# Kernel optimization log

Hardware: AMD Instinct MI355X
Metric: run time of the kernel (lower is better)

## Reference

```python
import jax, jax.numpy as jnp
import numpy as np

DIM = 512
CTX = 768
GROUPS = 32
EPS = 1e-5


def setup_inputs() -> dict:
    key = jax.random.key(0)
    ks = jax.random.split(key, 12)
    B, H, W, S = 16, 64, 64, 256
    x = jax.random.normal(ks[0], (B, DIM, H, W), dtype=jnp.float32)
    context = jax.random.normal(ks[1], (B, S, CTX), dtype=jnp.float32)
    gn_w = jnp.ones((DIM,), jnp.float32)
    gn_b = jnp.zeros((DIM,), jnp.float32)
    ln_w = jnp.ones((CTX,), jnp.float32)
    ln_b = jnp.zeros((CTX,), jnp.float32)
    wq = jax.random.normal(ks[2], (DIM, DIM), jnp.float32) * (DIM ** -0.5)
    bq = jnp.zeros((DIM,), jnp.float32)
    wkv = jax.random.normal(ks[3], (2 * DIM, CTX), jnp.float32) * (CTX ** -0.5)
    bkv = jnp.zeros((2 * DIM,), jnp.float32)
    wo = jax.random.normal(ks[4], (DIM, DIM), jnp.float32) * (DIM ** -0.5)
    bo = jnp.zeros((DIM,), jnp.float32)
    return {"x": x, "context": context, "gn_w": gn_w, "gn_b": gn_b,
            "ln_w": ln_w, "ln_b": ln_b, "wq": wq, "bq": bq,
            "wkv": wkv, "bkv": bkv, "wo": wo, "bo": bo}


def reference(x, context, gn_w, gn_b, ln_w, ln_b, wq, bq, wkv, bkv, wo, bo):
    b, c, h, w = x.shape
    scale = c ** -0.5
    # GroupNorm over (channels-per-group, H, W)
    xr = x.reshape(b, GROUPS, -1)
    mu = xr.mean(-1, keepdims=True)
    var = xr.var(-1, keepdims=True)
    xn = ((xr - mu) * jax.lax.rsqrt(var + EPS)).reshape(b, c, h, w)
    xn = xn * gn_w[None, :, None, None] + gn_b[None, :, None, None]
    # 1x1 conv query projection as channel GEMM
    q = jnp.einsum('bchw,oc->bohw', xn, wq) + bq[None, :, None, None]
    q = q.reshape(b, c, h * w).transpose(0, 2, 1)  # b, hw, c
    # LayerNorm on context
    cm = context.mean(-1, keepdims=True)
    cv = context.var(-1, keepdims=True)
    cn = (context - cm) * jax.lax.rsqrt(cv + EPS) * ln_w + ln_b
    kv = cn @ wkv.T + bkv  # b, s, 2c
    k, v = jnp.split(kv, 2, axis=-1)
    sim = jnp.einsum('bic,bjc->bij', q, k) * scale
    attn = jax.nn.softmax(sim, axis=-1)
    out = jnp.einsum('bij,bjc->bic', attn, v)
    out = out.transpose(0, 2, 1).reshape(b, c, h, w)
    out = jnp.einsum('bchw,oc->bohw', out, wo) + bo[None, :, None, None]
    return out + x
```

## Files before the change

### kernel.cpp

```cpp
#include <hip/hip_runtime.h>

typedef unsigned short u16;
typedef __attribute__((ext_vector_type(8))) short short8;
typedef __attribute__((ext_vector_type(4))) float f32x4;

#define DIM 512
#define CTX 768
#define HW 4096
#define NB 16
#define NS 256
#define EPSV 1e-5f

__device__ inline u16 f2bf(float f) {
    union { float f; unsigned u; } x; x.f = f;
    unsigned r = x.u + 0x7fffu + ((x.u >> 16) & 1u);
    return (u16)(r >> 16);
}
__device__ inline float bf2f(u16 v) {
    union { unsigned u; float f; } x; x.u = (unsigned)v << 16; return x.f;
}

__global__ void gn_stats(const float* __restrict__ x, const float* __restrict__ gn_w,
                         const float* __restrict__ gn_b, float* __restrict__ ga,
                         float* __restrict__ gd) {
    const int bg = blockIdx.x;
    const int b = bg >> 5, g = bg & 31;
    const float* base = x + ((long)b * DIM + g * 16) * HW;
    float s1 = 0.f, s2 = 0.f;
    const int tid = threadIdx.x;
    for (int i = tid; i < 16384; i += 256) {
        float4 v = ((const float4*)base)[i];
        s1 += v.x + v.y + v.z + v.w;
        s2 += v.x * v.x + v.y * v.y + v.z * v.z + v.w * v.w;
    }
    __shared__ float r1[256], r2[256];
    r1[tid] = s1; r2[tid] = s2; __syncthreads();
    for (int s = 128; s > 0; s >>= 1) {
        if (tid < s) { r1[tid] += r1[tid + s]; r2[tid] += r2[tid + s]; }
        __syncthreads();
    }
    __shared__ float mu_s, rs_s;
    if (tid == 0) {
        float mu = r1[0] * (1.f / 65536.f);
        float var = r2[0] * (1.f / 65536.f) - mu * mu;
        mu_s = mu; rs_s = rsqrtf(var + EPSV);
    }
    __syncthreads();
    if (tid < 16) {
        int c = g * 16 + tid;
        float aa = rs_s * gn_w[c];
        ga[b * DIM + c] = aa;
        gd[b * DIM + c] = gn_b[c] - mu_s * aa;
    }
}

__global__ void gn_apply_t(const float* __restrict__ x, const float* __restrict__ ga,
                           const float* __restrict__ gd, u16* __restrict__ xnt) {
    const int b = blockIdx.y;
    const int c0 = (blockIdx.x & 7) * 64;
    const int p0 = (blockIdx.x >> 3) * 64;
    __shared__ u16 t[64][68];
    const int tid = threadIdx.x;
    const int tc = tid >> 4;
    const int tp = (tid & 15) * 4;
    #pragma unroll
    for (int i = 0; i < 4; i++) {
        const int c = c0 + tc + i * 16;
        const float a = ga[b * DIM + c];
        const float d = gd[b * DIM + c];
        float4 v = *(const float4*)&x[((long)b * DIM + c) * HW + p0 + tp];
        u16* dst = &t[tc + i * 16][tp];
        dst[0] = f2bf(v.x * a + d);
        dst[1] = f2bf(v.y * a + d);
        dst[2] = f2bf(v.z * a + d);
        dst[3] = f2bf(v.w * a + d);
    }
    __syncthreads();
    const int wp = tid >> 3;
    const int wc = (tid & 7) * 8;
    #pragma unroll
    for (int i = 0; i < 2; i++) {
        const int p = wp + i * 32;
        short8 o;
        #pragma unroll
        for (int k = 0; k < 8; k++) o[k] = t[wc + k][p];
        *(short8*)&xnt[((long)b * HW + p0 + p) * DIM + c0 + wc] = o;
    }
}

__global__ void ln_ctx(const float* __restrict__ ctx, const float* __restrict__ ln_w,
                       const float* __restrict__ ln_b, u16* __restrict__ cn) {
    const int row = blockIdx.x;
    const int tid = threadIdx.x;
    const float* r = ctx + (long)row * CTX;
    float v[3]; float s1 = 0.f, s2 = 0.f;
    #pragma unroll
    for (int i = 0; i < 3; i++) { v[i] = r[tid + i * 256]; s1 += v[i]; s2 += v[i] * v[i]; }
    __shared__ float r1[256], r2[256];
    r1[tid] = s1; r2[tid] = s2; __syncthreads();
    for (int s = 128; s > 0; s >>= 1) {
        if (tid < s) { r1[tid] += r1[tid + s]; r2[tid] += r2[tid + s]; }
        __syncthreads();
    }
    __shared__ float mu_s, rs_s;
    if (tid == 0) {
        float mu = r1[0] * (1.f / 768.f);
        float var = r2[0] * (1.f / 768.f) - mu * mu;
        mu_s = mu; rs_s = rsqrtf(var + EPSV);
    }
    __syncthreads();
    #pragma unroll
    for (int i = 0; i < 3; i++) {
        int idx = tid + i * 256;
        cn[(long)row * CTX + idx] = f2bf((v[i] - mu_s) * rs_s * ln_w[idx] + ln_b[idx]);
    }
}

__global__ void cvt_weights(const float* __restrict__ wq, const float* __restrict__ wkv,
                            const float* __restrict__ wo, u16* __restrict__ wqtb,
                            u16* __restrict__ wkvb, u16* __restrict__ wob) {
    int i = blockIdx.x * 256 + threadIdx.x;
    if (i < 262144) {
        wqtb[(i & 511) * 512 + (i >> 9)] = f2bf(wq[i]);
        wob[i] = f2bf(wo[i]);
    }
    if (i < 786432) wkvb[i] = f2bf(wkv[i]);
}

__global__ void kbias_k(const u16* __restrict__ k, const float* __restrict__ bq,
                        float* __restrict__ kbias) {
    const int row = blockIdx.x;
    const int tid = threadIdx.x;
    const u16* r = k + (long)row * DIM;
    float s = bf2f(r[tid]) * bq[tid] + bf2f(r[tid + 256]) * bq[tid + 256];
    __shared__ float red[256];
    red[tid] = s; __syncthreads();
    for (int st = 128; st > 0; st >>= 1) {
        if (tid < st) red[tid] += red[tid + st];
        __syncthreads();
    }
    if (tid == 0) kbias[row] = red[0];
}

__launch_bounds__(256, 2)
__global__ void gemm_kv(const u16* __restrict__ A, const u16* __restrict__ Bm,
                        const float* __restrict__ bias,
                        u16* __restrict__ outk, u16* __restrict__ outv) {
    __shared__ u16 As[128][56];
    __shared__ u16 Bs[128][56];
    const int tid = threadIdx.x;
    const int lane = tid & 63;
    const int wave = tid >> 6;
    const int bb = blockIdx.y;
    const int m0 = (blockIdx.x >> 3) << 7;
    const int n0 = (blockIdx.x & 7) << 7;
    const u16* Ab = A + (long)bb * NS * CTX + (long)m0 * CTX;
    const u16* Bb = Bm + (long)n0 * CTX;

    const int sr = tid >> 2;
    const int sc = (tid & 3) << 3;
    const int l16 = lane & 15;
    const int quad = lane >> 4;
    const int wr = (wave >> 1) << 6;
    const int wc = (wave & 1) << 6;

    const u16* Ap0 = Ab + (long)sr * CTX + sc;
    const u16* Ap1 = Ab + (long)(sr + 64) * CTX + sc;
    const u16* Bp0 = Bb + (long)sr * CTX + sc;
    const u16* Bp1 = Bb + (long)(sr + 64) * CTX + sc;
    short8 rA0 = *(const short8*)Ap0;
    short8 rA1 = *(const short8*)Ap1;
    short8 rB0 = *(const short8*)Bp0;
    short8 rB1 = *(const short8*)Bp1;

    f32x4 acc[4][4] = {};
    for (int k0 = 0; k0 < CTX; k0 += 32) {
        if (k0) __syncthreads();
        *(short8*)&As[sr][sc]      = rA0;
        *(short8*)&As[sr + 64][sc] = rA1;
        *(short8*)&Bs[sr][sc]      = rB0;
        *(short8*)&Bs[sr + 64][sc] = rB1;
        __syncthreads();
        if (k0 + 32 < CTX) {
            rA0 = *(const short8*)(Ap0 + k0 + 32);
            rA1 = *(const short8*)(Ap1 + k0 + 32);
            rB0 = *(const short8*)(Bp0 + k0 + 32);
            rB1 = *(const short8*)(Bp1 + k0 + 32);
        }
        short8 af[4], bfr[4];
        #pragma unroll
        for (int i = 0; i < 4; i++) af[i] = *(const short8*)&As[wr + i * 16 + l16][quad * 8];
        #pragma unroll
        for (int j = 0; j < 4; j++) bfr[j] = *(const short8*)&Bs[wc + j * 16 + l16][quad * 8];
        #pragma unroll
        for (int i = 0; i < 4; i++)
            #pragma unroll
            for (int j = 0; j < 4; j++)
                acc[i][j] = __builtin_amdgcn_mfma_f32_16x16x32_bf16(af[i], bfr[j], acc[i][j], 0, 0, 0);
    }

    #pragma unroll
    for (int i = 0; i < 4; i++) {
        #pragma unroll
        for (int r = 0; r < 4; r++) {
            const int row = m0 + wr + i * 16 + quad * 4 + r;
            #pragma unroll
            for (int j = 0; j < 4; j++) {
                const int col = n0 + wc + j * 16 + l16;
                float v = acc[i][j][r] + bias[col];
                if (col < DIM) outk[(long)bb * NS * DIM + (long)row * DIM + col] = f2bf(v);
                else           outv[(long)bb * NS * DIM + (long)row * DIM + (col - DIM)] = f2bf(v);
            }
        }
    }
}

__launch_bounds__(256, 2)
__global__ void gemm_qv(const u16* __restrict__ kb_, const u16* __restrict__ vb_,
                        const u16* __restrict__ wqtb, const u16* __restrict__ wob,
                        u16* __restrict__ Kq, u16* __restrict__ Vot) {
    __shared__ u16 As[128][56];
    __shared__ u16 Bs[128][56];
    const int tid = threadIdx.x;
    const int lane = tid & 63;
    const int wave = tid >> 6;
    const int bb = blockIdx.y;
    const bool isV = blockIdx.z != 0;
    const int m0 = (blockIdx.x >> 2) << 7;
    const int n0 = (blockIdx.x & 3) << 7;
    const u16* Ab = (isV ? vb_ : kb_) + (long)bb * NS * DIM + (long)m0 * DIM;
    const u16* Bb = (isV ? wob : wqtb) + (long)n0 * DIM;

    const int sr = tid >> 2;
    const int sc = (tid & 3) << 3;
    const int l16 = lane & 15;
    const int quad = lane >> 4;
    const int wr = (wave >> 1) << 6;
    const int wc = (wave & 1) << 6;

    const u16* Ap0 = Ab + (long)sr * DIM + sc;
    const u16* Ap1 = Ab + (long)(sr + 64) * DIM + sc;
    const u16* Bp0 = Bb + (long)sr * DIM + sc;
    const u16* Bp1 = Bb + (long)(sr + 64) * DIM + sc;
    short8 rA0 = *(const short8*)Ap0;
    short8 rA1 = *(const short8*)Ap1;
    short8 rB0 = *(const short8*)Bp0;
    short8 rB1 = *(const short8*)Bp1;

    f32x4 acc[4][4] = {};
    for (int k0 = 0; k0 < DIM; k0 += 32) {
        if (k0) __syncthreads();
        *(short8*)&As[sr][sc]      = rA0;
        *(short8*)&As[sr + 64][sc] = rA1;
        *(short8*)&Bs[sr][sc]      = rB0;
        *(short8*)&Bs[sr + 64][sc] = rB1;
        __syncthreads();
        if (k0 + 32 < DIM) {
            rA0 = *(const short8*)(Ap0 + k0 + 32);
            rA1 = *(const short8*)(Ap1 + k0 + 32);
            rB0 = *(const short8*)(Bp0 + k0 + 32);
            rB1 = *(const short8*)(Bp1 + k0 + 32);
        }
        short8 af[4], bfr[4];
        #pragma unroll
        for (int i = 0; i < 4; i++) af[i] = *(const short8*)&As[wr + i * 16 + l16][quad * 8];
        #pragma unroll
        for (int j = 0; j < 4; j++) bfr[j] = *(const short8*)&Bs[wc + j * 16 + l16][quad * 8];
        #pragma unroll
        for (int i = 0; i < 4; i++)
            #pragma unroll
            for (int j = 0; j < 4; j++)
                acc[i][j] = __builtin_amdgcn_mfma_f32_16x16x32_bf16(af[i], bfr[j], acc[i][j], 0, 0, 0);
    }

    #pragma unroll
    for (int i = 0; i < 4; i++) {
        #pragma unroll
        for (int r = 0; r < 4; r++) {
            const int row = m0 + wr + i * 16 + quad * 4 + r;
            #pragma unroll
            for (int j = 0; j < 4; j++) {
                const int col = n0 + wc + j * 16 + l16;
                const u16 v = f2bf(acc[i][j][r]);
                if (!isV) Kq[(long)bb * NS * DIM + (long)row * DIM + col] = v;
                else      Vot[(long)bb * DIM * NS + (long)col * NS + row] = v;
            }
        }
    }
}

__launch_bounds__(512, 4)
__global__ void flash_attn(const u16* __restrict__ xnt, const u16* __restrict__ Kq,
                           const u16* __restrict__ Vot, const float* __restrict__ kbias,
                           const float* __restrict__ bo, const float* __restrict__ x,
                           float* __restrict__ out) {
    __shared__ __align__(16) char fsm[69632];
    u16 (*As)[56]      = (u16(*)[56])(fsm);
    u16 (*Bs)[56]      = (u16(*)[56])(fsm + 14336);
    u16 (*P)[264]      = (u16(*)[264])(fsm);
    float (*red)[4]    = (float(*)[4])(fsm + 67584);

    const int tid = threadIdx.x;
    const int lane = tid & 63;
    const int wave = tid >> 6;
    const int mw = wave >> 2;
    const int nw = wave & 3;
    const int l16 = lane & 15;
    const int quad = lane >> 4;
    const int b = blockIdx.y;
    const int m0 = blockIdx.x << 7;

    const u16* Ab = xnt + ((long)b * HW + m0) * DIM;
    const u16* Bb = Kq + (long)b * NS * DIM;

    const int rS = tid >> 2, cS = (tid & 3) << 3;
    const int rB = tid >> 1, cB = (tid & 1) << 4;
    const u16* Ap = Ab + (long)rS * DIM + cS;
    const u16* Bp = Bb + (long)rB * DIM + cB;
    short8 rA  = *(const short8*)(Ap);
    short8 rB0 = *(const short8*)(Bp);
    short8 rB1 = *(const short8*)(Bp + 8);

    f32x4 acc[4][4] = {};
    for (int k0 = 0; k0 < DIM; k0 += 32) {
        if (k0) __syncthreads();
        *(short8*)&As[rS][cS]     = rA;
        *(short8*)&Bs[rB][cB]     = rB0;
        *(short8*)&Bs[rB][cB + 8] = rB1;
        __syncthreads();
        if (k0 + 32 < DIM) {
            rA  = *(const short8*)(Ap + k0 + 32);
            rB0 = *(const short8*)(Bp + k0 + 32);
            rB1 = *(const short8*)(Bp + k0 + 40);
        }
        short8 af[4], bfr[4];
        #pragma unroll
        for (int i = 0; i < 4; i++) af[i] = *(const short8*)&As[mw * 64 + i * 16 + l16][quad * 8];
        #pragma unroll
        for (int j = 0; j < 4; j++) bfr[j] = *(const short8*)&Bs[nw * 64 + j * 16 + l16][quad * 8];
        #pragma unroll
        for (int i = 0; i < 4; i++)
            #pragma unroll
            for (int j = 0; j < 4; j++)
                acc[i][j] = __builtin_amdgcn_mfma_f32_16x16x32_bf16(af[i], bfr[j], acc[i][j], 0, 0, 0);
    }

    const float scale = 0.044194173824159216f;
    float kb[4];
    #pragma unroll
    for (int j = 0; j < 4; j++) kb[j] = kbias[b * NS + nw * 64 + j * 16 + l16];

    #pragma unroll
    for (int i = 0; i < 4; i++) {
        #pragma unroll
        for (int r = 0; r < 4; r++) {
            float m = -1e30f;
            #pragma unroll
            for (int j = 0; j < 4; j++) {
                float v = (acc[i][j][r] + kb[j]) * scale;
                acc[i][j][r] = v;
                m = fmaxf(m, v);
            }
            #pragma unroll
            for (int off = 1; off < 16; off <<= 1) m = fmaxf(m, __shfl_xor(m, off));
            if (l16 == 0) red[mw * 64 + i * 16 + quad * 4 + r][nw] = m;
        }
    }
    __syncthreads();
    float rsum[4][4];
    #pragma unroll
    for (int i = 0; i < 4; i++) {
        #pragma unroll
        for (int r = 0; r < 4; r++) {
            const int row = mw * 64 + i * 16 + quad * 4 + r;
            float4 rv = *(const float4*)red[row];
            float gm = fmaxf(fmaxf(rv.x, rv.y), fmaxf(rv.z, rv.w));
            float s = 0.f;
            #pragma unroll
            for (int j = 0; j < 4; j++) {
                float e = __expf(acc[i][j][r] - gm);
                acc[i][j][r] = e;
                s += e;
            }
            #pragma unroll
            for (int off = 1; off < 16; off <<= 1) s += __shfl_xor(s, off);
            rsum[i][r] = s;
        }
    }
    __syncthreads();
    #pragma unroll
    for (int i = 0; i < 4; i++)
        #pragma unroll
        for (int r = 0; r < 4; r++)
            if (l16 == 0) red[mw * 64 + i * 16 + quad * 4 + r][nw] = rsum[i][r];
    __syncthreads();
    #pragma unroll
    for (int i = 0; i < 4; i++) {
        #pragma unroll
        for (int r = 0; r < 4; r++) {
            const int row = mw * 64 + i * 16 + quad * 4 + r;
            float4 sv = *(const float4*)red[row];
            float inv = 1.f / (sv.x + sv.y + sv.z + sv.w);
            #pragma unroll
            for (int j = 0; j < 4; j++)
                P[row][nw * 64 + j * 16 + l16] = f2bf(acc[i][j][r] * inv);
        }
    }
    __syncthreads();

    const u16* Vb = Vot + ((long)b * DIM + nw * 32 + l16) * NS + quad * 8;
    for (int nc = 0; nc < 4; nc++) {
        f32x4 oacc[4][2];
        #pragma unroll
        for (int i = 0; i < 4; i++)
            #pragma unroll
            for (int jj = 0; jj < 2; jj++)
                oacc[i][jj] = (f32x4){0.f, 0.f, 0.f, 0.f};
        #pragma unroll
        for (int kk = 0; kk < 8; kk++) {
            short8 pf[4], vf[2];
            #pragma unroll
            for (int i = 0; i < 4; i++)
                pf[i] = *(const short8*)&P[mw * 64 + i * 16 + l16][kk * 32 + quad * 8];
            #pragma unroll
            for (int jj = 0; jj < 2; jj++)
                vf[jj] = *(const short8*)(Vb + (long)(nc * 128 + jj * 16) * NS + kk * 32);
            #pragma unroll
            for (int i = 0; i < 4; i++)
                #pragma unroll
                for (int jj = 0; jj < 2; jj++)
                    oacc[i][jj] = __builtin_amdgcn_mfma_f32_16x16x32_bf16(pf[i], vf[jj], oacc[i][jj], 0, 0, 0);
        }
        #pragma unroll
        for (int jj = 0; jj < 2; jj++) {
            const int c = nc * 128 + nw * 32 + jj * 16 + l16;
            const float bv = bo[c];
            const long base = ((long)b * DIM + c) * HW + m0 + mw * 64 + quad * 4;
            #pragma unroll
            for (int i = 0; i < 4; i++) {
                float4 xv = *(const float4*)&x[base + i * 16];
                float4 o;
                o.x = oacc[i][jj][0] + xv.x + bv;
                o.y = oacc[i][jj][1] + xv.y + bv;
                o.z = oacc[i][jj][2] + xv.z + bv;
                o.w = oacc[i][jj][3] + xv.w + bv;
                *(float4*)&out[base + i * 16] = o;
            }
        }
    }
}

extern "C" void kernel_launch(void* const* d_in, const int* in_sizes, int n_in,
                              void* d_out, int out_size, void* d_ws, size_t ws_size,
                              hipStream_t stream) {
    const float* x    = (const float*)d_in[0];
    const float* ctx  = (const float*)d_in[1];
    const float* gn_w = (const float*)d_in[2];
    const float* gn_b = (const float*)d_in[3];
    const float* ln_w = (const float*)d_in[4];
    const float* ln_b = (const float*)d_in[5];
    const float* wq   = (const float*)d_in[6];
    const float* bq   = (const float*)d_in[7];
    const float* wkv  = (const float*)d_in[8];
    const float* bkv  = (const float*)d_in[9];
    const float* wo   = (const float*)d_in[10];
    const float* bo   = (const float*)d_in[11];

    char* ws = (char*)d_ws;
    u16*   xnt  = (u16*)(ws + 0);
    u16*   cn   = (u16*)(ws + 67108864);
    u16*   kb_  = (u16*)(ws + 73400320);
    u16*   vb_  = (u16*)(ws + 77594624);
    u16*   Kq   = (u16*)(ws + 81788928);
    u16*   Vot  = (u16*)(ws + 85983232);
    u16*   wqtb = (u16*)(ws + 90177536);
    u16*   wkvb = (u16*)(ws + 90701824);
    u16*   wob  = (u16*)(ws + 92274688);
    float* ga   = (float*)(ws + 92798976);
    float* gd   = ga + NB * DIM;
    float* kbias = (float*)(ws + 92864512);

    gn_stats<<<dim3(NB * 32), dim3(256), 0, stream>>>(x, gn_w, gn_b, ga, gd);
    gn_apply_t<<<dim3(512, NB), dim3(256), 0, stream>>>(x, ga, gd, xnt);
    ln_ctx<<<dim3(NB * NS), dim3(256), 0, stream>>>(ctx, ln_w, ln_b, cn);
    cvt_weights<<<dim3(3072), dim3(256), 0, stream>>>(wq, wkv, wo, wqtb, wkvb, wob);

    gemm_kv<<<dim3(2 * 8, NB), dim3(256), 0, stream>>>(cn, wkvb, bkv, kb_, vb_);
    gemm_qv<<<dim3(2 * 4, NB, 2), dim3(256), 0, stream>>>(kb_, vb_, wqtb, wob, Kq, Vot);
    kbias_k<<<dim3(NB * NS), dim3(256), 0, stream>>>(kb_, bq, kbias);
    flash_attn<<<dim3(32, NB), dim3(512), 0, stream>>>(
        xnt, Kq, Vot, kbias, bo, x, (float*)d_out);
}
```

Measured before the change: 450.7 us.

## Fold Wq/Wo into KV weights and restage attention epilogue through LDS

```diff
diff --git a/kernel.cpp b/kernel.cpp
--- a/kernel.cpp
+++ b/kernel.cpp
@@ -88,8 +88,55 @@
     }
 }
 
+__global__ void cvt_weights(const float* __restrict__ wq, const float* __restrict__ wkv,
+                            const float* __restrict__ wo, u16* __restrict__ wqtb,
+                            u16* __restrict__ wkvtb, u16* __restrict__ wob) {
+    int i = blockIdx.x * 256 + threadIdx.x;
+    if (i < 262144) {
+        wqtb[(i & 511) * 512 + (i >> 9)] = f2bf(wq[i]);
+        wob[i] = f2bf(wo[i]);
+    }
+    if (i < 786432) {
+        int o = i / 768, e = i - o * 768;
+        wkvtb[e * 1024 + o] = f2bf(wkv[i]);
+    }
+}
+
+__global__ void bias_prep(const u16* __restrict__ wqtb, const u16* __restrict__ wob,
+                          const u16* __restrict__ wkvtb, const float* __restrict__ bq,
+                          const float* __restrict__ bkv, float* __restrict__ bKV,
+                          float* __restrict__ wt, float* __restrict__ c0) {
+    const int bid = blockIdx.x, tid = threadIdx.x;
+    float s = 0.f;
+    if (bid < 512) {
+        const u16* r = wqtb + (long)bid * 512;
+        s = bf2f(r[tid]) * bkv[tid] + bf2f(r[tid + 256]) * bkv[tid + 256];
+    } else if (bid < 1024) {
+        const u16* r = wob + (long)(bid - 512) * 512;
+        s = bf2f(r[tid]) * bkv[512 + tid] + bf2f(r[tid + 256]) * bkv[512 + tid + 256];
+    } else if (bid < 1792) {
+        const u16* r = wkvtb + (long)(bid - 1024) * 1024;
+        s = bf2f(r[tid]) * bq[tid] + bf2f(r[tid + 256]) * bq[tid + 256];
+    } else {
+        s = bq[tid] * bkv[tid] + bq[tid + 256] * bkv[tid + 256];
+    }
+    __shared__ float red[256];
+    red[tid] = s; __syncthreads();
+    for (int st = 128; st > 0; st >>= 1) {
+        if (tid < st) red[tid] += red[tid + st];
+        __syncthreads();
+    }
+    if (tid == 0) {
+        if (bid < 1024) bKV[bid] = red[0];
+        else if (bid < 1792) wt[bid - 1024] = red[0];
+        else *c0 = red[0];
+    }
+}
+
 __global__ void ln_ctx(const float* __restrict__ ctx, const float* __restrict__ ln_w,
-                       const float* __restrict__ ln_b, u16* __restrict__ cn) {
+                       const float* __restrict__ ln_b, const float* __restrict__ wt,
+                       const float* __restrict__ c0, u16* __restrict__ cn,
+                       float* __restrict__ kbias) {
     const int row = blockIdx.x;
     const int tid = threadIdx.x;
     const float* r = ctx + (long)row * CTX;
@@ -109,43 +156,95 @@
         mu_s = mu; rs_s = rsqrtf(var + EPSV);
     }
     __syncthreads();
+    float kb = 0.f;
     #pragma unroll
     for (int i = 0; i < 3; i++) {
         int idx = tid + i * 256;
-        cn[(long)row * CTX + idx] = f2bf((v[i] - mu_s) * rs_s * ln_w[idx] + ln_b[idx]);
-    }
-}
-
-__global__ void cvt_weights(const float* __restrict__ wq, const float* __restrict__ wkv,
-                            const float* __restrict__ wo, u16* __restrict__ wqtb,
-                            u16* __restrict__ wkvb, u16* __restrict__ wob) {
-    int i = blockIdx.x * 256 + threadIdx.x;
-    if (i < 262144) {
-        wqtb[(i & 511) * 512 + (i >> 9)] = f2bf(wq[i]);
-        wob[i] = f2bf(wo[i]);
-    }
-    if (i < 786432) wkvb[i] = f2bf(wkv[i]);
-}
-
-__global__ void kbias_k(const u16* __restrict__ k, const float* __restrict__ bq,
-                        float* __restrict__ kbias) {
-    const int row = blockIdx.x;
+        float nv = (v[i] - mu_s) * rs_s * ln_w[idx] + ln_b[idx];
+        cn[(long)row * CTX + idx] = f2bf(nv);
+        kb += nv * wt[idx];
+    }
+    r1[tid] = kb; __syncthreads();
+    for (int s = 128; s > 0; s >>= 1) {
+        if (tid < s) r1[tid] += r1[tid + s];
+        __syncthreads();
+    }
+    if (tid == 0) kbias[row] = r1[0] + *c0;
+}
+
+__launch_bounds__(256, 2)
+__global__ void gemm_wprep(const u16* __restrict__ wqtb, const u16* __restrict__ wob,
+                           const u16* __restrict__ wkvtb, u16* __restrict__ Wt) {
+    __shared__ u16 As[128][56];
+    __shared__ u16 Bs[128][56];
     const int tid = threadIdx.x;
-    const u16* r = k + (long)row * DIM;
-    float s = bf2f(r[tid]) * bq[tid] + bf2f(r[tid + 256]) * bq[tid + 256];
-    __shared__ float red[256];
-    red[tid] = s; __syncthreads();
-    for (int st = 128; st > 0; st >>= 1) {
-        if (tid < st) red[tid] += red[tid + st];
-        __syncthreads();
-    }
-    if (tid == 0) kbias[row] = red[0];
+    const int lane = tid & 63;
+    const int wave = tid >> 6;
+    const bool isV = blockIdx.z != 0;
+    const int m0 = (blockIdx.x / 6) << 7;
+    const int n0 = (blockIdx.x % 6) << 7;
+    const u16* Ab = (isV ? wob : wqtb) + (long)m0 * 512;
+    const u16* Bb = wkvtb + (long)n0 * 1024 + (isV ? 512 : 0);
+    u16* Ob = Wt + (isV ? (long)512 * 768 : 0);
+
+    const int sr = tid >> 2;
+    const int sc = (tid & 3) << 3;
+    const int l16 = lane & 15;
+    const int quad = lane >> 4;
+    const int wr = (wave >> 1) << 6;
+    const int wc = (wave & 1) << 6;
+
+    const u16* Ap0 = Ab + (long)sr * 512 + sc;
+    const u16* Ap1 = Ab + (long)(sr + 64) * 512 + sc;
+    const u16* Bp0 = Bb + (long)sr * 1024 + sc;
+    const u16* Bp1 = Bb + (long)(sr + 64) * 1024 + sc;
+    short8 rA0 = *(const short8*)Ap0;
+    short8 rA1 = *(const short8*)Ap1;
+    short8 rB0 = *(const short8*)Bp0;
+    short8 rB1 = *(const short8*)Bp1;
+
+    f32x4 acc[4][4] = {};
+    for (int k0 = 0; k0 < 512; k0 += 32) {
+        if (k0) __syncthreads();
+        *(short8*)&As[sr][sc]      = rA0;
+        *(short8*)&As[sr + 64][sc] = rA1;
+        *(short8*)&Bs[sr][sc]      = rB0;
+        *(short8*)&Bs[sr + 64][sc] = rB1;
+        __syncthreads();
+        if (k0 + 32 < 512) {
+            rA0 = *(const short8*)(Ap0 + k0 + 32);
+            rA1 = *(const short8*)(Ap1 + k0 + 32);
+            rB0 = *(const short8*)(Bp0 + k0 + 32);
+            rB1 = *(const short8*)(Bp1 + k0 + 32);
+        }
+        short8 af[4], bfr[4];
+        #pragma unroll
+        for (int i = 0; i < 4; i++) af[i] = *(const short8*)&As[wr + i * 16 + l16][quad * 8];
+        #pragma unroll
+        for (int j = 0; j < 4; j++) bfr[j] = *(const short8*)&Bs[wc + j * 16 + l16][quad * 8];
+        #pragma unroll
+        for (int i = 0; i < 4; i++)
+            #pragma unroll
+            for (int j = 0; j < 4; j++)
+                acc[i][j] = __builtin_amdgcn_mfma_f32_16x16x32_bf16(af[i], bfr[j], acc[i][j], 0, 0, 0);
+    }
+    #pragma unroll
+    for (int i = 0; i < 4; i++)
+        #pragma unroll
+        for (int r = 0; r < 4; r++) {
+            const int row = m0 + wr + i * 16 + quad * 4 + r;
+            #pragma unroll
+            for (int j = 0; j < 4; j++) {
+                const int col = n0 + wc + j * 16 + l16;
+                Ob[(long)row * 768 + col] = f2bf(acc[i][j][r]);
+            }
+        }
 }
 
 __launch_bounds__(256, 2)
-__global__ void gemm_kv(const u16* __restrict__ A, const u16* __restrict__ Bm,
-                        const float* __restrict__ bias,
-                        u16* __restrict__ outk, u16* __restrict__ outv) {
+__global__ void gemm_kvq(const u16* __restrict__ cn, const u16* __restrict__ Wt,
+                         const float* __restrict__ bKV,
+                         u16* __restrict__ Kq, u16* __restrict__ Vot) {
     __shared__ u16 As[128][56];
     __shared__ u16 Bs[128][56];
     const int tid = threadIdx.x;
@@ -154,8 +253,8 @@
     const int bb = blockIdx.y;
     const int m0 = (blockIdx.x >> 3) << 7;
     const int n0 = (blockIdx.x & 7) << 7;
-    const u16* Ab = A + (long)bb * NS * CTX + (long)m0 * CTX;
-    const u16* Bb = Bm + (long)n0 * CTX;
+    const u16* Ab = cn + (long)bb * NS * CTX + (long)m0 * CTX;
+    const u16* Bb = Wt + (long)n0 * CTX;
 
     const int sr = tid >> 2;
     const int sc = (tid & 3) << 3;
@@ -200,93 +299,18 @@
     }
 
     #pragma unroll
-    for (int i = 0; i < 4; i++) {
+    for (int i = 0; i < 4; i++)
         #pragma unroll
         for (int r = 0; r < 4; r++) {
             const int row = m0 + wr + i * 16 + quad * 4 + r;
             #pragma unroll
             for (int j = 0; j < 4; j++) {
                 const int col = n0 + wc + j * 16 + l16;
-                float v = acc[i][j][r] + bias[col];
-                if (col < DIM) outk[(long)bb * NS * DIM + (long)row * DIM + col] = f2bf(v);
-                else           outv[(long)bb * NS * DIM + (long)row * DIM + (col - DIM)] = f2bf(v);
+                const u16 v = f2bf(acc[i][j][r] + bKV[col]);
+                if (col < DIM) Kq[(long)bb * NS * DIM + (long)row * DIM + col] = v;
+                else           Vot[(long)bb * DIM * NS + (long)(col - DIM) * NS + row] = v;
             }
         }
-    }
-}
-
-__launch_bounds__(256, 2)
-__global__ void gemm_qv(const u16* __restrict__ kb_, const u16* __restrict__ vb_,
-                        const u16* __restrict__ wqtb, const u16* __restrict__ wob,
-                        u16* __restrict__ Kq, u16* __restrict__ Vot) {
-    __shared__ u16 As[128][56];
-    __shared__ u16 Bs[128][56];
-    const int tid = threadIdx.x;
-    const int lane = tid & 63;
-    const int wave = tid >> 6;
-    const int bb = blockIdx.y;
-    const bool isV = blockIdx.z != 0;
-    const int m0 = (blockIdx.x >> 2) << 7;
-    const int n0 = (blockIdx.x & 3) << 7;
-    const u16* Ab = (isV ? vb_ : kb_) + (long)bb * NS * DIM + (long)m0 * DIM;
-    const u16* Bb = (isV ? wob : wqtb) + (long)n0 * DIM;
-
-    const int sr = tid >> 2;
-    const int sc = (tid & 3) << 3;
-    const int l16 = lane & 15;
-    const int quad = lane >> 4;
-    const int wr = (wave >> 1) << 6;
-    const int wc = (wave & 1) << 6;
-
-    const u16* Ap0 = Ab + (long)sr * DIM + sc;
-    const u16* Ap1 = Ab + (long)(sr + 64) * DIM + sc;
-    const u16* Bp0 = Bb + (long)sr * DIM + sc;
-    const u16* Bp1 = Bb + (long)(sr + 64) * DIM + sc;
-    short8 rA0 = *(const short8*)Ap0;
-    short8 rA1 = *(const short8*)Ap1;
-    short8 rB0 = *(const short8*)Bp0;
-    short8 rB1 = *(const short8*)Bp1;
-
-    f32x4 acc[4][4] = {};
-    for (int k0 = 0; k0 < DIM; k0 += 32) {
-        if (k0) __syncthreads();
-        *(short8*)&As[sr][sc]      = rA0;
-        *(short8*)&As[sr + 64][sc] = rA1;
-        *(short8*)&Bs[sr][sc]      = rB0;
-        *(short8*)&Bs[sr + 64][sc] = rB1;
-        __syncthreads();
-        if (k0 + 32 < DIM) {
-            rA0 = *(const short8*)(Ap0 + k0 + 32);
-            rA1 = *(const short8*)(Ap1 + k0 + 32);
-            rB0 = *(const short8*)(Bp0 + k0 + 32);
-            rB1 = *(const short8*)(Bp1 + k0 + 32);
-        }
-        short8 af[4], bfr[4];
-        #pragma unroll
-        for (int i = 0; i < 4; i++) af[i] = *(const short8*)&As[wr + i * 16 + l16][quad * 8];
-        #pragma unroll
-        for (int j = 0; j < 4; j++) bfr[j] = *(const short8*)&Bs[wc + j * 16 + l16][quad * 8];
-        #pragma unroll
-        for (int i = 0; i < 4; i++)
-            #pragma unroll
-            for (int j = 0; j < 4; j++)
-                acc[i][j] = __builtin_amdgcn_mfma_f32_16x16x32_bf16(af[i], bfr[j], acc[i][j], 0, 0, 0);
-    }
-
-    #pragma unroll
-    for (int i = 0; i < 4; i++) {
-        #pragma unroll
-        for (int r = 0; r < 4; r++) {
-            const int row = m0 + wr + i * 16 + quad * 4 + r;
-            #pragma unroll
-            for (int j = 0; j < 4; j++) {
-                const int col = n0 + wc + j * 16 + l16;
-                const u16 v = f2bf(acc[i][j][r]);
-                if (!isV) Kq[(long)bb * NS * DIM + (long)row * DIM + col] = v;
-                else      Vot[(long)bb * DIM * NS + (long)col * NS + row] = v;
-            }
-        }
-    }
 }
 
 __launch_bounds__(512, 4)
@@ -294,11 +318,12 @@
                            const u16* __restrict__ Vot, const float* __restrict__ kbias,
                            const float* __restrict__ bo, const float* __restrict__ x,
                            float* __restrict__ out) {
-    __shared__ __align__(16) char fsm[69632];
+    __shared__ __align__(16) char fsm[78080];
     u16 (*As)[56]      = (u16(*)[56])(fsm);
     u16 (*Bs)[56]      = (u16(*)[56])(fsm + 14336);
     u16 (*P)[264]      = (u16(*)[264])(fsm);
     float (*red)[4]    = (float(*)[4])(fsm + 67584);
+    float (*lbuf)[132] = (float(*)[132])(fsm + 69632);
 
     const int tid = threadIdx.x;
     const int lane = tid & 63;
@@ -432,19 +457,27 @@
                     oacc[i][jj] = __builtin_amdgcn_mfma_f32_16x16x32_bf16(pf[i], vf[jj], oacc[i][jj], 0, 0, 0);
         }
         #pragma unroll
-        for (int jj = 0; jj < 2; jj++) {
-            const int c = nc * 128 + nw * 32 + jj * 16 + l16;
-            const float bv = bo[c];
-            const long base = ((long)b * DIM + c) * HW + m0 + mw * 64 + quad * 4;
-            #pragma unroll
-            for (int i = 0; i < 4; i++) {
-                float4 xv = *(const float4*)&x[base + i * 16];
-                float4 o;
-                o.x = oacc[i][jj][0] + xv.x + bv;
-                o.y = oacc[i][jj][1] + xv.y + bv;
-                o.z = oacc[i][jj][2] + xv.z + bv;
-                o.w = oacc[i][jj][3] + xv.w + bv;
-                *(float4*)&out[base + i * 16] = o;
+        for (int t = 0; t < 8; t++) {
+            __syncthreads();
+            if (nw == (t >> 1)) {
+                const int jj = t & 1;
+                #pragma unroll
+                for (int i = 0; i < 4; i++)
+                    #pragma unroll
+                    for (int r = 0; r < 4; r++)
+                        lbuf[l16][mw * 64 + i * 16 + quad * 4 + r] = oacc[i][jj][r];
+            }
+            __syncthreads();
+            {
+                const int cl = tid >> 5;
+                const int p4 = (tid & 31) * 4;
+                const int cg = nc * 128 + t * 16 + cl;
+                const long idx = ((long)b * DIM + cg) * HW + m0 + p4;
+                const float bv = bo[cg];
+                float4 v0 = *(const float4*)&lbuf[cl][p4];
+                float4 x0 = *(const float4*)&x[idx];
+                v0.x += x0.x + bv; v0.y += x0.y + bv; v0.z += x0.z + bv; v0.w += x0.w + bv;
+                *(float4*)&out[idx] = v0;
             }
         }
     }
@@ -467,27 +500,28 @@
     const float* bo   = (const float*)d_in[11];
 
     char* ws = (char*)d_ws;
-    u16*   xnt  = (u16*)(ws + 0);
-    u16*   cn   = (u16*)(ws + 67108864);
-    u16*   kb_  = (u16*)(ws + 73400320);
-    u16*   vb_  = (u16*)(ws + 77594624);
-    u16*   Kq   = (u16*)(ws + 81788928);
-    u16*   Vot  = (u16*)(ws + 85983232);
-    u16*   wqtb = (u16*)(ws + 90177536);
-    u16*   wkvb = (u16*)(ws + 90701824);
-    u16*   wob  = (u16*)(ws + 92274688);
-    float* ga   = (float*)(ws + 92798976);
-    float* gd   = ga + NB * DIM;
-    float* kbias = (float*)(ws + 92864512);
+    u16*   xnt   = (u16*)(ws + 0);
+    u16*   cn    = (u16*)(ws + 67108864);
+    u16*   Kq    = (u16*)(ws + 73400320);
+    u16*   Vot   = (u16*)(ws + 77594624);
+    u16*   wqtb  = (u16*)(ws + 81788928);
+    u16*   wob   = (u16*)(ws + 82313216);
+    u16*   wkvtb = (u16*)(ws + 82837504);
+    u16*   Wt    = (u16*)(ws + 84410368);
+    float* bKV   = (float*)(ws + 85983232);
+    float* wt    = (float*)(ws + 85987328);
+    float* c0    = (float*)(ws + 85990400);
+    float* ga    = (float*)(ws + 85991424);
+    float* gd    = ga + NB * DIM;
+    float* kbias = (float*)(ws + 86056960);
 
     gn_stats<<<dim3(NB * 32), dim3(256), 0, stream>>>(x, gn_w, gn_b, ga, gd);
     gn_apply_t<<<dim3(512, NB), dim3(256), 0, stream>>>(x, ga, gd, xnt);
-    ln_ctx<<<dim3(NB * NS), dim3(256), 0, stream>>>(ctx, ln_w, ln_b, cn);
-    cvt_weights<<<dim3(3072), dim3(256), 0, stream>>>(wq, wkv, wo, wqtb, wkvb, wob);
-
-    gemm_kv<<<dim3(2 * 8, NB), dim3(256), 0, stream>>>(cn, wkvb, bkv, kb_, vb_);
-    gemm_qv<<<dim3(2 * 4, NB, 2), dim3(256), 0, stream>>>(kb_, vb_, wqtb, wob, Kq, Vot);
-    kbias_k<<<dim3(NB * NS), dim3(256), 0, stream>>>(kb_, bq, kbias);
+    cvt_weights<<<dim3(3072), dim3(256), 0, stream>>>(wq, wkv, wo, wqtb, wkvtb, wob);
+    bias_prep<<<dim3(1793), dim3(256), 0, stream>>>(wqtb, wob, wkvtb, bq, bkv, bKV, wt, c0);
+    ln_ctx<<<dim3(NB * NS), dim3(256), 0, stream>>>(ctx, ln_w, ln_b, wt, c0, cn, kbias);
+    gemm_wprep<<<dim3(24, 1, 2), dim3(256), 0, stream>>>(wqtb, wob, wkvtb, Wt);
+    gemm_kvq<<<dim3(2 * 8, NB), dim3(256), 0, stream>>>(cn, Wt, bKV, Kq, Vot);
     flash_attn<<<dim3(32, NB), dim3(512), 0, stream>>>(
         xnt, Kq, Vot, kbias, bo, x, (float*)d_out);
 }
```

Measured after the change: 421.6 us. 1.07x faster.
